# Optimization experiments

Measured on AMD Instinct MI355X. Metric: run time of the kernel, lower is better.

Reference implementation:

```python
import jax, jax.numpy as jnp
import numpy as np

D, BEV_H, BEV_W, NH, NP = 256, 200, 200, 8, 8
NQ = BEV_H * BEV_W
DFF = 1024
HD = D // NH


def setup_inputs() -> dict:
    key = jax.random.key(0)
    ks = jax.random.split(key, 12)
    def rn(k, shape, scale=0.02):
        return jax.random.normal(k, shape, jnp.float32) * scale
    return dict(
        B_adj0=rn(ks[0], (1, NQ, D), 1.0),
        B_adj1=rn(ks[1], (1, NQ, D), 1.0),
        query_embed=rn(ks[2], (NQ, D), 1.0),
        W_ref=rn(ks[3], (D, 2)), b_ref=jnp.zeros((2,), jnp.float32),
        W_off=rn(ks[4], (D, NH * NP * 2)), b_off=rn(ks[5], (NH * NP * 2,), 0.5),
        W_attn=rn(ks[6], (D, NH * NP)), b_attn=jnp.zeros((NH * NP,), jnp.float32),
        W_val=rn(ks[7], (D, D)), b_val=jnp.zeros((D,), jnp.float32),
        W_out=rn(ks[8], (D, D)), b_out=jnp.zeros((D,), jnp.float32),
        W_ffn1=rn(ks[9], (D, DFF)), b_ffn1=jnp.zeros((DFF,), jnp.float32),
        W_ffn2=rn(ks[10], (DFF, D)), b_ffn2=jnp.zeros((D,), jnp.float32),
    )


def _deform_attend(value, loc, attn_w):
    """Bilinear-sample `value` (bs,NQ,NH,HD laid out as BEV_H x BEV_W map) at
    normalized locations loc (bs,nq,NH,NP,2) with align_corners=False and zero
    padding (torch grid_sample semantics), weighted by attn_w (bs,nq,NH,NP)."""
    bs, _, nh, hd = value.shape
    nq = loc.shape[1]
    vt = value.transpose(0, 2, 1, 3)  # (bs, nh, HW, hd)
    # grid = 2*loc - 1 ; pixel = ((grid+1)*size - 1)/2 = loc*size - 0.5
    x = loc[..., 0] * BEV_W - 0.5
    y = loc[..., 1] * BEV_H - 0.5
    x0f = jnp.floor(x); y0f = jnp.floor(y)
    lx = x - x0f; ly = y - y0f
    x0 = x0f.astype(jnp.int32); y0 = y0f.astype(jnp.int32)
    acc = jnp.zeros((bs, nh, nq, hd), value.dtype)
    corners = ((0, 0, (1 - lx) * (1 - ly)), (1, 0, lx * (1 - ly)),
               (0, 1, (1 - lx) * ly), (1, 1, lx * ly))
    for dx, dy, w in corners:
        ix = x0 + dx
        iy = y0 + dy
        valid = ((ix >= 0) & (ix < BEV_W) & (iy >= 0) & (iy < BEV_H)).astype(value.dtype)
        idx = jnp.clip(iy, 0, BEV_H - 1) * BEV_W + jnp.clip(ix, 0, BEV_W - 1)  # (bs,nq,nh,np)
        idx_t = idx.transpose(0, 2, 1, 3).reshape(bs, nh, nq * NP)
        v = jnp.take_along_axis(vt, idx_t[..., None], axis=2).reshape(bs, nh, nq, NP, hd)
        wt = (w * valid * attn_w).transpose(0, 2, 1, 3)  # (bs,nh,nq,np)
        acc = acc + (wt[..., None] * v).sum(3)
    return acc.transpose(0, 2, 1, 3).reshape(bs, nq, nh * hd)


def reference(B_adj0, B_adj1, query_embed, W_ref, b_ref, W_off, b_off,
              W_attn, b_attn, W_val, b_val, W_out, b_out,
              W_ffn1, b_ffn1, W_ffn2, b_ffn2):
    bs = B_adj0.shape[0]
    q = jnp.broadcast_to(query_embed[None], (bs, NQ, D))
    # reference points in [0,1]
    ref = jax.nn.sigmoid(q @ W_ref + b_ref)  # (bs,nq,2)
    off = (q @ W_off + b_off).reshape(bs, NQ, NH, NP, 2)
    attn = jax.nn.softmax((q @ W_attn + b_attn).reshape(bs, NQ, NH, NP), axis=-1)
    offset_normalizer = jnp.array([BEV_W, BEV_H], jnp.float32)
    loc = ref[:, :, None, None, :] + off / offset_normalizer  # (bs,nq,nh,np,2)
    B_short = jnp.zeros((bs, NQ, D), B_adj0.dtype)
    for V in (B_adj0, B_adj1):
        val = (V @ W_val + b_val).reshape(bs, NQ, NH, HD)
        out = _deform_attend(val, loc, attn) @ W_out + b_out
        B_short = B_short + out + q  # mmcv MSDA residual: identity = query
    # FFN with residual (mmcv FFN, add_identity=True, drop=0)
    ffn = jax.nn.relu(B_short @ W_ffn1 + b_ffn1) @ W_ffn2 + b_ffn2
    return B_short + ffn
```

## Files before the change

### kernel.cpp

```cpp
#include <hip/hip_runtime.h>
#include <hip/hip_bf16.h>

#define NQ    40000
#define DD    256
#define NHH   8
#define NPP   8
#define DFF   1024
#define BEV   200
#define MPAD  40064

typedef __attribute__((ext_vector_type(4))) float f32x4;
typedef __attribute__((ext_vector_type(8))) short s16x8;
typedef __hip_bfloat16 bf16;

#define AS1(p) ((const __attribute__((address_space(1))) void*)(p))
#define AS3(p) ((__attribute__((address_space(3))) void*)(p))

__device__ inline unsigned short f2bf(float f) {
  union { bf16 h; unsigned short u; } cv;
  cv.h = __float2bfloat16(f);
  return cv.u;
}
__device__ inline float bf2f(bf16 h) { return __bfloat162float(h); }
__device__ inline float bfs(short u) {
  union { float f; unsigned u; } c;
  c.u = ((unsigned)(unsigned short)u) << 16;
  return c.f;
}

__global__ void transpose_cvt(const float* __restrict__ src, bf16* __restrict__ dst,
                              int R, int C) {
  int i = blockIdx.x * 256 + threadIdx.x;
  if (i >= R * C) return;
  int c = i / R, r = i % R;
  dst[i] = __float2bfloat16(src[(size_t)r * C + c]);
}

__global__ void build_wq(const float* __restrict__ Woff, const float* __restrict__ Wattn,
                         const float* __restrict__ Wref, bf16* __restrict__ dst) {
  int i = blockIdx.x * 256 + threadIdx.x;
  int n = i >> 8, k = i & 255;
  float v;
  if (n < 128)      v = Woff[k * 128 + n];
  else if (n < 192) v = Wattn[k * 64 + (n - 128)];
  else if (n < 194) v = Wref[k * 2 + (n - 192)];
  else              v = 0.f;
  dst[i] = __float2bfloat16(v);
}

__global__ void cvt_bf16_kernel(const float* __restrict__ src, bf16* __restrict__ dst, int n4) {
  int i = blockIdx.x * 256 + threadIdx.x;
  if (i >= n4) return;
  float4 v = ((const float4*)src)[i];
  ushort4 o;
  o.x = f2bf(v.x); o.y = f2bf(v.y); o.z = f2bf(v.z); o.w = f2bf(v.w);
  ((ushort4*)dst)[i] = o;
}

__global__ void addcvt_kernel(const float* __restrict__ a, const float* __restrict__ b,
                              bf16* __restrict__ dst, int n4) {
  int i = blockIdx.x * 256 + threadIdx.x;
  if (i >= n4) return;
  float4 va = ((const float4*)a)[i];
  float4 vb = ((const float4*)b)[i];
  ushort4 o;
  o.x = f2bf(va.x + vb.x); o.y = f2bf(va.y + vb.y);
  o.z = f2bf(va.z + vb.z); o.w = f2bf(va.w + vb.w);
  ((ushort4*)dst)[i] = o;
}

template<bool RELU>
__global__ void gemm_bt(const bf16* __restrict__ A, const bf16* __restrict__ Bt,
                        int K, int Ntiles, int N,
                        const float* __restrict__ bias, float biasScale,
                        const float* __restrict__ addF, float addScale,
                        bf16* __restrict__ outB, float* __restrict__ outF, int Mvalid) {
  __shared__ __align__(16) char smem[32768];
  const int tid  = threadIdx.x;
  const int wave = tid >> 6, lane = tid & 63;
  const int tm = blockIdx.x / Ntiles, tn = blockIdx.x % Ntiles;
  const int wr = wave >> 1, wc = wave & 1;

  f32x4 acc[4][4];
#pragma unroll
  for (int i = 0; i < 4; ++i)
#pragma unroll
    for (int j = 0; j < 4; ++j) {
      f32x4 z = {0.f, 0.f, 0.f, 0.f};
      acc[i][j] = z;
    }

  const char* Ab = (const char*)A;
  const char* Bb = (const char*)Bt;
  const int nK = K >> 6;

  for (int kt = 0; kt < nK; ++kt) {
#pragma unroll
    for (int i = 0; i < 8; ++i) {
      const int j  = wave * 8 + i;
      const int p0 = j << 10;
      const char* g;
      if (p0 < 16384) {
        const int pl = p0 + lane * 16;
        const int row = pl >> 7, cb = pl & 127;
        g = Ab + ((size_t)(tm * 128 + row) * K + kt * 64) * 2 + cb;
      } else {
        const int pl = p0 - 16384 + lane * 16;
        const int row = pl >> 7, cb = pl & 127;
        g = Bb + ((size_t)(tn * 128 + row) * K + kt * 64) * 2 + cb;
      }
      __builtin_amdgcn_global_load_lds(AS1(g), AS3(smem + p0), 16, 0, 0);
    }
    __syncthreads();

#pragma unroll
    for (int kk = 0; kk < 2; ++kk) {
      const int r  = lane & 15;
      const int kb = kk * 64 + (lane >> 4) * 16;
      s16x8 af[4], bfr[4];
#pragma unroll
      for (int mr = 0; mr < 4; ++mr)
        af[mr] = *(const s16x8*)(smem + (wr * 64 + mr * 16 + r) * 128 + kb);
#pragma unroll
      for (int nr = 0; nr < 4; ++nr)
        bfr[nr] = *(const s16x8*)(smem + 16384 + (wc * 64 + nr * 16 + r) * 128 + kb);
#pragma unroll
      for (int mr = 0; mr < 4; ++mr)
#pragma unroll
        for (int nr = 0; nr < 4; ++nr)
          acc[mr][nr] = __builtin_amdgcn_mfma_f32_16x16x32_bf16(af[mr], bfr[nr], acc[mr][nr], 0, 0, 0);
    }
    __syncthreads();
  }

  const int r = lane & 15, rg = lane >> 4;
#pragma unroll
  for (int mr = 0; mr < 4; ++mr) {
#pragma unroll
    for (int nr = 0; nr < 4; ++nr) {
      const int gn = tn * 128 + wc * 64 + nr * 16 + r;
      const float bval = bias ? biasScale * bias[gn] : 0.f;
#pragma unroll
      for (int j2 = 0; j2 < 4; ++j2) {
        const int gm = tm * 128 + wr * 64 + mr * 16 + rg * 4 + j2;
        float v = acc[mr][nr][j2] + bval;
        if (addF && gm < Mvalid) v += addScale * addF[(size_t)gm * N + gn];
        if (RELU) v = fmaxf(v, 0.f);
        if (outB) outB[(size_t)gm * N + gn] = __float2bfloat16(v);
        if (outF && gm < Mvalid) outF[(size_t)gm * N + gn] = v;
      }
    }
  }
}

__global__ void finalize_kernel(const bf16* __restrict__ raw, const float* __restrict__ b_off,
                                const float* __restrict__ b_attn, const float* __restrict__ b_ref,
                                float* __restrict__ samp) {
  __shared__ float r[4][256];
  const int tid = threadIdx.x;
  const int q0 = blockIdx.x * 4;
#pragma unroll
  for (int i = 0; i < 4; ++i) {
    int e = tid + i * 256;
    int ql = e >> 8, k = e & 255;
    r[ql][k] = bf2f(raw[(size_t)(q0 + ql) * 256 + k]);
  }
  __syncthreads();
  const int ql = tid >> 6, hp = tid & 63;
  const int h = hp >> 3, p = hp & 7;
  float v[8];
  float m = -1e30f;
#pragma unroll
  for (int pp = 0; pp < 8; ++pp) {
    v[pp] = r[ql][128 + h * 8 + pp] + b_attn[h * 8 + pp];
    m = fmaxf(m, v[pp]);
  }
  float s = 0.f;
#pragma unroll
  for (int pp = 0; pp < 8; ++pp) { v[pp] = expf(v[pp] - m); s += v[pp]; }
  const float w = v[p] / s;
  const float sx = 1.f / (1.f + expf(-(r[ql][192] + b_ref[0])));
  const float sy = 1.f / (1.f + expf(-(r[ql][193] + b_ref[1])));
  const float px = sx * (float)BEV + (r[ql][hp * 2 + 0] + b_off[hp * 2 + 0]) - 0.5f;
  const float py = sy * (float)BEV + (r[ql][hp * 2 + 1] + b_off[hp * 2 + 1]) - 0.5f;
  const size_t o = ((size_t)(q0 + ql) * 64 + hp) * 3;
  samp[o] = px; samp[o + 1] = py; samp[o + 2] = w;
}

__global__ __launch_bounds__(256, 4)
void deform_kernel(const float* __restrict__ samp, const bf16* __restrict__ val,
                   bf16* __restrict__ out) {
  __shared__ float s[8 * 192];
  const int tid = threadIdx.x;
  const int q0 = blockIdx.x * 8;
#pragma unroll
  for (int i = 0; i < 6; ++i) {
    const int e = tid + i * 256;
    s[e] = samp[(size_t)q0 * 192 + e];
  }
  __syncthreads();
  const int ql = tid >> 5;
  const int lane5 = tid & 31;
  const int h = lane5 >> 2;
  const int dg = lane5 & 3;
  const float* sp = s + ql * 192 + h * 24;
  const bf16* vb = val + h * 32 + dg * 8;

  float acc[8] = {0.f, 0.f, 0.f, 0.f, 0.f, 0.f, 0.f, 0.f};
#pragma unroll 2
  for (int p = 0; p < 8; ++p) {
    const float px = sp[p * 3 + 0], py = sp[p * 3 + 1], w = sp[p * 3 + 2];
    const float xf = floorf(px), yf = floorf(py);
    const int x0 = (int)xf, y0 = (int)yf;
    const float lx = px - xf, ly = py - yf;
    const float xa = (x0 >= 0 && x0 < BEV) ? 1.f : 0.f;
    const float xb = (x0 + 1 >= 0 && x0 + 1 < BEV) ? 1.f : 0.f;
    const float ya = (y0 >= 0 && y0 < BEV) ? 1.f : 0.f;
    const float yb = (y0 + 1 >= 0 && y0 + 1 < BEV) ? 1.f : 0.f;
    const float w00 = w * (1.f - lx) * (1.f - ly) * xa * ya;
    const float w10 = w * lx * (1.f - ly) * xb * ya;
    const float w01 = w * (1.f - lx) * ly * xa * yb;
    const float w11 = w * lx * ly * xb * yb;
    const int cx0 = min(max(x0, 0), BEV - 1);
    const int cx1 = min(max(x0 + 1, 0), BEV - 1);
    const int cy0 = min(max(y0, 0), BEV - 1) * BEV;
    const int cy1 = min(max(y0 + 1, 0), BEV - 1) * BEV;
    const s16x8 v00 = *(const s16x8*)(vb + (size_t)(cy0 + cx0) * 256);
    const s16x8 v10 = *(const s16x8*)(vb + (size_t)(cy0 + cx1) * 256);
    const s16x8 v01 = *(const s16x8*)(vb + (size_t)(cy1 + cx0) * 256);
    const s16x8 v11 = *(const s16x8*)(vb + (size_t)(cy1 + cx1) * 256);
#pragma unroll
    for (int j = 0; j < 8; ++j) {
      acc[j] += w00 * bfs(v00[j]) + w10 * bfs(v10[j])
              + w01 * bfs(v01[j]) + w11 * bfs(v11[j]);
    }
  }
  s16x8 o;
#pragma unroll
  for (int j = 0; j < 8; ++j) o[j] = (short)f2bf(acc[j]);
  *(s16x8*)(out + (size_t)(q0 + ql) * 256 + h * 32 + dg * 8) = o;
}

extern "C" void kernel_launch(void* const* d_in, const int* in_sizes, int n_in,
                              void* d_out, int out_size, void* d_ws, size_t ws_size,
                              hipStream_t stream) {
  const float* B0     = (const float*)d_in[0];
  const float* B1     = (const float*)d_in[1];
  const float* qe     = (const float*)d_in[2];
  const float* W_ref  = (const float*)d_in[3];
  const float* b_ref  = (const float*)d_in[4];
  const float* W_off  = (const float*)d_in[5];
  const float* b_off  = (const float*)d_in[6];
  const float* W_attn = (const float*)d_in[7];
  const float* b_attn = (const float*)d_in[8];
  const float* W_val  = (const float*)d_in[9];
  const float* b_val  = (const float*)d_in[10];
  const float* W_out  = (const float*)d_in[11];
  const float* b_out  = (const float*)d_in[12];
  const float* W_ffn1 = (const float*)d_in[13];
  const float* b_ffn1 = (const float*)d_in[14];
  const float* W_ffn2 = (const float*)d_in[15];
  const float* b_ffn2 = (const float*)d_in[16];
  float* out = (float*)d_out;
  char* ws = (char*)d_ws;

  const size_t SZ_MAT = (size_t)MPAD * 256 * 2;
  const size_t VAL_OFF    = 0;
  const size_t RAW_OFF    = SZ_MAT;
  const size_t BSH_OFF    = 2 * SZ_MAT;
  const size_t H_OFF      = 3 * SZ_MAT;
  const size_t QE_OFF     = H_OFF;
  const size_t VSUM_OFF   = H_OFF + SZ_MAT;
  const size_t H_BYTES    = (size_t)MPAD * 1024 * 2;
  const size_t SAMP_OFF   = H_OFF + H_BYTES;
  const size_t SAMP_BYTES = (size_t)NQ * 192 * 4;
  const size_t WQ_OFF     = SAMP_OFF + SAMP_BYTES;
  const size_t WVAL_OFF   = WQ_OFF   + 256 * 256 * 2;
  const size_t WOUT_OFF   = WVAL_OFF + 256 * 256 * 2;
  const size_t WF1_OFF    = WOUT_OFF + 256 * 256 * 2;
  const size_t WF2_OFF    = WF1_OFF  + 1024 * 256 * 2;

  bf16* valb  = (bf16*)(ws + VAL_OFF);
  bf16* rawb  = (bf16*)(ws + RAW_OFF);
  bf16* defb  = rawb;
  bf16* bshb  = (bf16*)(ws + BSH_OFF);
  bf16* hbuf  = (bf16*)(ws + H_OFF);
  bf16* qeb   = (bf16*)(ws + QE_OFF);
  bf16* vsum  = (bf16*)(ws + VSUM_OFF);
  float* samp = (float*)(ws + SAMP_OFF);
  bf16* wq    = (bf16*)(ws + WQ_OFF);
  bf16* wval  = (bf16*)(ws + WVAL_OFF);
  bf16* wout  = (bf16*)(ws + WOUT_OFF);
  bf16* wf1   = (bf16*)(ws + WF1_OFF);
  bf16* wf2   = (bf16*)(ws + WF2_OFF);

  const int n4 = NQ * 256 / 4;
  const int MT = MPAD / 128;

  build_wq<<<256, 256, 0, stream>>>(W_off, W_attn, W_ref, wq);
  transpose_cvt<<<(256 * 256 + 255) / 256, 256, 0, stream>>>(W_val, wval, 256, 256);
  transpose_cvt<<<(256 * 256 + 255) / 256, 256, 0, stream>>>(W_out, wout, 256, 256);
  transpose_cvt<<<(256 * 1024 + 255) / 256, 256, 0, stream>>>(W_ffn1, wf1, 256, 1024);
  transpose_cvt<<<(1024 * 256 + 255) / 256, 256, 0, stream>>>(W_ffn2, wf2, 1024, 256);

  cvt_bf16_kernel<<<n4 / 256, 256, 0, stream>>>(qe, qeb, n4);
  addcvt_kernel<<<n4 / 256, 256, 0, stream>>>(B0, B1, vsum, n4);

  gemm_bt<false><<<MT * 2, 256, 0, stream>>>(qeb, wq, 256, 2, 256,
                                             nullptr, 0.f, nullptr, 0.f,
                                             rawb, nullptr, NQ);
  finalize_kernel<<<NQ / 4, 256, 0, stream>>>(rawb, b_off, b_attn, b_ref, samp);

  gemm_bt<false><<<MT * 2, 256, 0, stream>>>(vsum, wval, 256, 2, 256,
                                             b_val, 2.f, nullptr, 0.f,
                                             valb, nullptr, NQ);

  deform_kernel<<<NQ / 8, 256, 0, stream>>>(samp, valb, defb);

  gemm_bt<false><<<MT * 2, 256, 0, stream>>>(defb, wout, 256, 2, 256,
                                             b_out, 2.f, qe, 2.f,
                                             bshb, out, NQ);

  gemm_bt<true><<<MT * 8, 256, 0, stream>>>(bshb, wf1, 256, 8, 1024,
                                            b_ffn1, 1.f, nullptr, 0.f,
                                            hbuf, nullptr, NQ);

  gemm_bt<false><<<MT * 2, 256, 0, stream>>>(hbuf, wf2, 1024, 2, 256,
                                             b_ffn2, 1.f, out, 1.f,
                                             nullptr, out, NQ);
}
```

Measured before the change: 313.1 us.

## Double-buffer GEMM LDS tiles, remap blocks per XCD, use bf16 residuals

The GEMM now holds two LDS buffers and issues global-to-LDS loads for the next K tile while MFMAs run on the current one. This removes one barrier per iteration and lets loads overlap compute, at the cost of twice the LDS per block. Block indices are remapped so consecutive tiles land on the same XCD, which should improve L2 reuse. The residual inputs are read as bf16 (qeb, bshb) instead of fp32, and the out-projection no longer writes an fp32 intermediate. This cuts memory traffic but drops residual precision to bf16.

```diff
diff --git a/kernel.cpp b/kernel.cpp
--- a/kernel.cpp
+++ b/kernel.cpp
@@ -70,15 +70,21 @@
 }
 
 template<bool RELU>
-__global__ void gemm_bt(const bf16* __restrict__ A, const bf16* __restrict__ Bt,
-                        int K, int Ntiles, int N,
-                        const float* __restrict__ bias, float biasScale,
-                        const float* __restrict__ addF, float addScale,
-                        bf16* __restrict__ outB, float* __restrict__ outF, int Mvalid) {
-  __shared__ __align__(16) char smem[32768];
+__global__ __launch_bounds__(256, 2)
+void gemm_bt(const bf16* __restrict__ A, const bf16* __restrict__ Bt,
+             int K, int Ntiles, int N,
+             const float* __restrict__ bias, float biasScale,
+             const bf16* __restrict__ addB, float addScale,
+             bf16* __restrict__ outB, float* __restrict__ outF, int Mvalid) {
+  __shared__ __align__(16) char smem[65536];
   const int tid  = threadIdx.x;
   const int wave = tid >> 6, lane = tid & 63;
-  const int tm = blockIdx.x / Ntiles, tn = blockIdx.x % Ntiles;
+  const int nwg = gridDim.x;
+  const int orig = blockIdx.x;
+  const int q8 = nwg >> 3, r8 = nwg & 7;
+  const int xcd = orig & 7, idx = orig >> 3;
+  const int wg = (xcd < r8 ? xcd * (q8 + 1) : r8 * (q8 + 1) + (xcd - r8) * q8) + idx;
+  const int tm = wg / Ntiles, tn = wg % Ntiles;
   const int wr = wave >> 1, wc = wave & 1;
 
   f32x4 acc[4][4];
@@ -94,7 +100,7 @@
   const char* Bb = (const char*)Bt;
   const int nK = K >> 6;
 
-  for (int kt = 0; kt < nK; ++kt) {
+  auto stage = [&](int bufBase, int kt) {
 #pragma unroll
     for (int i = 0; i < 8; ++i) {
       const int j  = wave * 8 + i;
@@ -109,10 +115,16 @@
         const int row = pl >> 7, cb = pl & 127;
         g = Bb + ((size_t)(tn * 128 + row) * K + kt * 64) * 2 + cb;
       }
-      __builtin_amdgcn_global_load_lds(AS1(g), AS3(smem + p0), 16, 0, 0);
-    }
-    __syncthreads();
-
+      __builtin_amdgcn_global_load_lds(AS1(g), AS3(smem + bufBase + p0), 16, 0, 0);
+    }
+  };
+
+  stage(0, 0);
+  __syncthreads();
+  int cur = 0;
+  for (int kt = 0; kt < nK; ++kt) {
+    if (kt + 1 < nK) stage((cur ^ 1) * 32768, kt + 1);
+    const char* sbuf = smem + cur * 32768;
 #pragma unroll
     for (int kk = 0; kk < 2; ++kk) {
       const int r  = lane & 15;
@@ -120,10 +132,10 @@
       s16x8 af[4], bfr[4];
 #pragma unroll
       for (int mr = 0; mr < 4; ++mr)
-        af[mr] = *(const s16x8*)(smem + (wr * 64 + mr * 16 + r) * 128 + kb);
+        af[mr] = *(const s16x8*)(sbuf + (wr * 64 + mr * 16 + r) * 128 + kb);
 #pragma unroll
       for (int nr = 0; nr < 4; ++nr)
-        bfr[nr] = *(const s16x8*)(smem + 16384 + (wc * 64 + nr * 16 + r) * 128 + kb);
+        bfr[nr] = *(const s16x8*)(sbuf + 16384 + (wc * 64 + nr * 16 + r) * 128 + kb);
 #pragma unroll
       for (int mr = 0; mr < 4; ++mr)
 #pragma unroll
@@ -131,6 +143,7 @@
           acc[mr][nr] = __builtin_amdgcn_mfma_f32_16x16x32_bf16(af[mr], bfr[nr], acc[mr][nr], 0, 0, 0);
     }
     __syncthreads();
+    cur ^= 1;
   }
 
   const int r = lane & 15, rg = lane >> 4;
@@ -144,7 +157,7 @@
       for (int j2 = 0; j2 < 4; ++j2) {
         const int gm = tm * 128 + wr * 64 + mr * 16 + rg * 4 + j2;
         float v = acc[mr][nr][j2] + bval;
-        if (addF && gm < Mvalid) v += addScale * addF[(size_t)gm * N + gn];
+        if (addB && gm < Mvalid) v += addScale * bf2f(addB[(size_t)gm * N + gn]);
         if (RELU) v = fmaxf(v, 0.f);
         if (outB) outB[(size_t)gm * N + gn] = __float2bfloat16(v);
         if (outF && gm < Mvalid) outF[(size_t)gm * N + gn] = v;
@@ -318,14 +331,14 @@
   deform_kernel<<<NQ / 8, 256, 0, stream>>>(samp, valb, defb);
 
   gemm_bt<false><<<MT * 2, 256, 0, stream>>>(defb, wout, 256, 2, 256,
-                                             b_out, 2.f, qe, 2.f,
-                                             bshb, out, NQ);
+                                             b_out, 2.f, qeb, 2.f,
+                                             bshb, nullptr, NQ);
 
   gemm_bt<true><<<MT * 8, 256, 0, stream>>>(bshb, wf1, 256, 8, 1024,
                                             b_ffn1, 1.f, nullptr, 0.f,
                                             hbuf, nullptr, NQ);
 
   gemm_bt<false><<<MT * 2, 256, 0, stream>>>(hbuf, wf2, 1024, 2, 256,
-                                             b_ffn2, 1.f, out, 1.f,
+                                             b_ffn2, 1.f, bshb, 1.f,
                                              nullptr, out, NQ);
 }
```

Result: slower. 341.6 us (+9.1%).
